# Kernel optimization log

Measured on AMD Instinct MI355X. Metric: run time of the kernel, lower is better.

Reference implementation:

```python
import jax, jax.numpy as jnp
import numpy as np

NUM_HEADS = 4

def setup_inputs() -> dict:
    key = jax.random.key(0)
    ks = jax.random.split(key, 5)
    B, N, C = 2, 4096, 256
    s = 0.02
    return {
        "x": jax.random.normal(ks[0], (B, N, C), dtype=jnp.float32),
        "qkv_w": jax.random.normal(ks[1], (3 * C, C), dtype=jnp.float32) * s,
        "qkv_b": jax.random.normal(ks[2], (3 * C,), dtype=jnp.float32) * s,
        "out_w": jax.random.normal(ks[3], (C, C), dtype=jnp.float32) * s,
        "out_b": jax.random.normal(ks[4], (C,), dtype=jnp.float32) * s,
    }

def reference(x, qkv_w, qkv_b, out_w, out_b):
    # x: [B, N, C]; manual multi-head self-attention (eval mode, dropout off)
    B, N, C = x.shape
    H = NUM_HEADS
    D = C // H
    qkv = x @ qkv_w.T + qkv_b                      # [B, N, 3C]
    qkv = qkv.reshape(B, N, 3, H, D)
    qkv = jnp.transpose(qkv, (2, 0, 3, 1, 4))      # [3, B, H, N, D]
    q, k, v = qkv[0], qkv[1], qkv[2]
    scale = D ** -0.5
    attn = jnp.einsum('bhnd,bhmd->bhnm', q, k) * scale  # [B, H, N, N]
    attn = jax.nn.softmax(attn, axis=-1)
    out = jnp.einsum('bhnm,bhmd->bhnd', attn, v)   # [B, H, N, D]
    out = jnp.transpose(out, (0, 2, 1, 3)).reshape(B, N, C)
    return out @ out_w.T + out_b
```

## Files before the change

### kernel.cpp

```cpp
#include <hip/hip_runtime.h>

typedef __bf16 bf16x8 __attribute__((ext_vector_type(8)));
typedef float f32x4 __attribute__((ext_vector_type(4)));

#define MFMA_BF16(a, b, c) __builtin_amdgcn_mfma_f32_16x16x32_bf16((a), (b), (c), 0, 0, 0)

#define C1 0.18033688f

static __device__ __forceinline__ unsigned short f2bf(float f) {
    unsigned int u = __float_as_uint(f);
    unsigned int r = (u + 0x7fffu + ((u >> 16) & 1u)) >> 16;
    return (unsigned short)r;
}
static __device__ __forceinline__ float bf2f(unsigned short us) {
    return __uint_as_float(((unsigned int)us) << 16);
}
static __device__ __forceinline__ float exp2_hw(float x) {
    float r;
    asm("v_exp_f32 %0, %1" : "=v"(r) : "v"(x));
    return r;
}
static __device__ __forceinline__ unsigned pack_rh(float a, float b) {
    return __byte_perm(__float_as_uint(a) + 0x8000u, __float_as_uint(b) + 0x8000u, 0x7632);
}
static __device__ __forceinline__ void gload16(const void* g, void* l) {
    __builtin_amdgcn_global_load_lds(
        (const __attribute__((address_space(1))) unsigned int*)g,
        (__attribute__((address_space(3))) unsigned int*)l, 16, 0, 0);
}

static __device__ __forceinline__ void conv_seg(const void* src, unsigned short* dst, int n,
                                                int lb, bool f32) {
#pragma unroll
    for (int j = 0; j < 4; j++) {
        int idx = lb * 1024 + j * 256 + (int)threadIdx.x;
        if (idx < n) {
            dst[idx] = f32 ? f2bf(((const float*)src)[idx]) : ((const unsigned short*)src)[idx];
        }
    }
}

__global__ __launch_bounds__(256) void convert_kernel(
    const void* __restrict__ x, const void* __restrict__ qw, const void* __restrict__ qb,
    const void* __restrict__ ow, const void* __restrict__ ob,
    unsigned short* __restrict__ xb, unsigned short* __restrict__ qwb,
    unsigned short* __restrict__ qbb, unsigned short* __restrict__ owb,
    unsigned short* __restrict__ obb, int* __restrict__ flag) {
    __shared__ int tot;
    if (threadIdx.x == 0) tot = 0;
    __syncthreads();
    {
        unsigned short v = ((const unsigned short*)x)[threadIdx.x];
        int e = (v >> 7) & 0xFF;
        if (e >= 195) atomicAdd(&tot, 1);
    }
    __syncthreads();
    const bool f32 = (tot >= 8);
    if (blockIdx.x == 0 && threadIdx.x == 0) flag[0] = f32 ? 1 : 0;

    const int bid = blockIdx.x;
    if (bid < 2048)       conv_seg(x,  xb,  2097152, bid,        f32);
    else if (bid < 2240)  conv_seg(qw, qwb, 196608,  bid - 2048, f32);
    else if (bid < 2241)  conv_seg(qb, qbb, 768,     bid - 2240, f32);
    else if (bid < 2305)  conv_seg(ow, owb, 65536,   bid - 2241, f32);
    else                  conv_seg(ob, obb, 256,     bid - 2305, f32);
}

template <int BM, bool QKV>
__global__ __launch_bounds__(256) void gemm_kernel(
    const unsigned short* __restrict__ A, const unsigned short* __restrict__ W,
    const unsigned short* __restrict__ bias, unsigned short* __restrict__ Cb,
    float* __restrict__ Cf, const int* __restrict__ flag,
    unsigned short* __restrict__ Vt, int Nout) {
    constexpr int K = 256;
    constexpr int WPM = BM / 64;
    constexpr int IA = BM / 32;
    constexpr int ABYT = BM * 128;
    __shared__ __align__(16) char sm[2 * ABYT + 16384];

    const int tid = threadIdx.x;
    const int lane = tid & 63;
    const int wv = tid >> 6;
    const int m16 = lane & 15;
    const int quad = lane >> 4;
    const int bm = blockIdx.x * BM;
    const int bn = blockIdx.y * 64;

    int ago[IA], alo[IA];
#pragma unroll
    for (int i = 0; i < IA; i++) {
        const int c = wv * (IA * 64) + i * 64 + lane;
        const int r = c >> 3, g = (c & 7) ^ (r & 7);
        ago[i] = r * (K * 2) + g * 16;
        alo[i] = c * 16;
    }
    int bgo[2], blo[2];
#pragma unroll
    for (int i = 0; i < 2; i++) {
        const int c = wv * 128 + i * 64 + lane;
        const int r = c >> 3, g = (c & 7) ^ (r & 7);
        bgo[i] = r * (K * 2) + g * 16;
        blo[i] = c * 16;
    }
    int aro[WPM][2], bro[4][2];
#pragma unroll
    for (int mb = 0; mb < WPM; mb++)
#pragma unroll
        for (int ks = 0; ks < 2; ks++) {
            const int row = wv * (WPM * 16) + mb * 16 + m16;
            aro[mb][ks] = row * 64 + ((4 * ks + quad) ^ (m16 & 7)) * 8;
        }
#pragma unroll
    for (int t = 0; t < 4; t++)
#pragma unroll
        for (int ks = 0; ks < 2; ks++) {
            const int row = t * 16 + m16;
            bro[t][ks] = row * 64 + ((4 * ks + quad) ^ (m16 & 7)) * 8;
        }

    const char* ag = (const char*)(A + (size_t)bm * K);
    const char* bg = (const char*)(W + (size_t)bn * K);

#pragma unroll
    for (int i = 0; i < IA; i++) gload16(ag + ago[i], sm + alo[i]);
#pragma unroll
    for (int i = 0; i < 2; i++) gload16(bg + bgo[i], sm + 2 * ABYT + blo[i]);

    f32x4 acc[WPM][4] = {};
#pragma unroll
    for (int kb = 0; kb < 4; kb++) {
        __syncthreads();
        const int cur = kb & 1;
        if (kb < 3) {
            ag += 128;
            bg += 128;
            char* Adst = sm + (cur ^ 1) * ABYT;
            char* Bdst = sm + 2 * ABYT + (cur ^ 1) * 8192;
#pragma unroll
            for (int i = 0; i < IA; i++) gload16(ag + ago[i], Adst + alo[i]);
#pragma unroll
            for (int i = 0; i < 2; i++) gload16(bg + bgo[i], Bdst + blo[i]);
        }
        const unsigned short* Alds = (const unsigned short*)(sm + cur * ABYT);
        const unsigned short* Blds = (const unsigned short*)(sm + 2 * ABYT + cur * 8192);
#pragma unroll
        for (int ks = 0; ks < 2; ks++) {
            bf16x8 bfr[4];
#pragma unroll
            for (int t = 0; t < 4; t++) bfr[t] = *(const bf16x8*)(Blds + bro[t][ks]);
#pragma unroll
            for (int mb = 0; mb < WPM; mb++) {
                const bf16x8 af = *(const bf16x8*)(Alds + aro[mb][ks]);
#pragma unroll
                for (int t = 0; t < 4; t++) acc[mb][t] = MFMA_BF16(af, bfr[t], acc[mb][t]);
            }
        }
    }

    const bool outf = (!QKV) && (flag != nullptr) && (*flag != 0);
#pragma unroll
    for (int mb = 0; mb < WPM; mb++) {
        const int row0 = bm + wv * (WPM * 16) + mb * 16 + quad * 4;
#pragma unroll
        for (int t = 0; t < 4; t++) {
            const int col = bn + t * 16 + m16;
            const float bv = bf2f(bias[col]);
            float v[4];
#pragma unroll
            for (int r = 0; r < 4; r++) v[r] = acc[mb][t][r] + bv;
            if (QKV) {
                if (col < 256) {
#pragma unroll
                    for (int r = 0; r < 4; r++)
                        Cb[(size_t)(row0 + r) * 768 + col] = f2bf(v[r] * C1);
                } else if (col < 512) {
#pragma unroll
                    for (int r = 0; r < 4; r++)
                        Cb[(size_t)(row0 + r) * 768 + col] = f2bf(v[r]);
                } else {
                    const int hh = (col - 512) >> 6, d = (col - 512) & 63;
                    const int bb = row0 >> 12, n0 = row0 & 4095;
                    uint2 w2;
                    w2.x = pack_rh(v[0], v[1]);
                    w2.y = pack_rh(v[2], v[3]);
                    *(uint2*)&Vt[((size_t)((bb * 4 + hh) * 64 + d)) * 4096 + n0] = w2;
                }
            } else {
                if (outf) {
#pragma unroll
                    for (int r = 0; r < 4; r++) Cf[(size_t)(row0 + r) * Nout + col] = v[r];
                } else {
#pragma unroll
                    for (int r = 0; r < 4; r++) Cb[(size_t)(row0 + r) * Nout + col] = f2bf(v[r]);
                }
            }
        }
    }
}

__global__ __launch_bounds__(256) void attn_kernel(
    const unsigned short* __restrict__ qkv, const unsigned short* __restrict__ Vt,
    unsigned short* __restrict__ attn, unsigned short* __restrict__ Opart,
    float* __restrict__ ml, int nsplit, int iters) {
    const int N = 4096, C3 = 768;
    __shared__ __align__(16) char sm[65536];

    const int tid = threadIdx.x;
    const int lane = tid & 63;
    const int wv = tid >> 6;
    const int m16 = lane & 15;
    const int quad = lane >> 4;

    const int bh = blockIdx.x & 7;
    const int qt = (blockIdx.x >> 3) & 63;
    const int kvs = blockIdx.x >> 9;
    const int b = bh >> 2, h = bh & 3;

    bf16x8 qf[4][2];
#pragma unroll
    for (int j = 0; j < 4; j++)
#pragma unroll
        for (int ks = 0; ks < 2; ks++)
            qf[j][ks] = *(const bf16x8*)(qkv + ((size_t)b * N + qt * 64 + j * 16 + m16) * C3 +
                                         h * 64 + ks * 32 + quad * 8);

    int kgo[4], vgo[4], klo[4], vlo[4];
#pragma unroll
    for (int i = 0; i < 4; i++) {
        const int c = wv * 256 + i * 64 + lane;
        const int r = c >> 3, g = (c & 7) ^ (r & 7);
        kgo[i] = r * 1536 + g * 16;
        klo[i] = c * 16;
        const int d = c >> 4, gg = (c & 15) ^ (d & 15);
        vgo[i] = d * 8192 + gg * 16;
        vlo[i] = c * 16;
    }
    int kro[2][2], vro[4], pwo[2][4], pro[4];
#pragma unroll
    for (int mb = 0; mb < 2; mb++)
#pragma unroll
        for (int ks = 0; ks < 2; ks++) {
            const int row = wv * 32 + mb * 16 + m16;
            kro[mb][ks] = row * 64 + ((4 * ks + quad) ^ (m16 & 7)) * 8;
        }
#pragma unroll
    for (int t = 0; t < 4; t++) vro[t] = (t * 16 + m16) * 128 + ((wv * 4 + quad) ^ m16) * 8;
#pragma unroll
    for (int mb = 0; mb < 2; mb++)
#pragma unroll
        for (int j = 0; j < 4; j++)
            pwo[mb][j] = wv * 2048 + (j * 16 + m16) * 32 +
                         ((2 * mb + (quad >> 1)) ^ (m16 & 3)) * 8 + (quad & 1) * 4;
#pragma unroll
    for (int j = 0; j < 4; j++)
        pro[j] = wv * 2048 + (j * 16 + m16) * 32 + (quad ^ (m16 & 3)) * 8;

    const char* kgp = (const char*)(qkv + (size_t)b * N * C3 + 256 + h * 64) +
                      (size_t)(kvs * iters) * 128 * 1536;
    const char* vgp = (const char*)(Vt + (size_t)bh * 64 * N) + (size_t)(kvs * iters) * 256;

#pragma unroll
    for (int i = 0; i < 4; i++) {
        gload16(kgp + kgo[i], sm + klo[i]);
        gload16(vgp + vgo[i], sm + 32768 + vlo[i]);
    }

    f32x4 o[4][4] = {};
    float lac[4] = {0.f, 0.f, 0.f, 0.f};

    for (int kt = 0; kt < iters; ++kt) {
        __syncthreads();
        const int cur = kt & 1;
        if (kt + 1 < iters) {
            kgp += 128 * 1536;
            vgp += 256;
            char* Kdst = sm + (cur ^ 1) * 16384;
            char* Vdst = sm + 32768 + (cur ^ 1) * 16384;
#pragma unroll
            for (int i = 0; i < 4; i++) {
                gload16(kgp + kgo[i], Kdst + klo[i]);
                gload16(vgp + vgo[i], Vdst + vlo[i]);
            }
        }
        unsigned short* Kb = (unsigned short*)(sm + cur * 16384);
        const unsigned short* Vb = (const unsigned short*)(sm + 32768 + cur * 16384);

        f32x4 s[2][4] = {};
#pragma unroll
        for (int mb = 0; mb < 2; mb++)
#pragma unroll
            for (int ks = 0; ks < 2; ks++) {
                const bf16x8 ka = *(const bf16x8*)(Kb + kro[mb][ks]);
#pragma unroll
                for (int j = 0; j < 4; j++) s[mb][j] = MFMA_BF16(ka, qf[j][ks], s[mb][j]);
            }

#pragma unroll
        for (int mb = 0; mb < 2; mb++)
#pragma unroll
            for (int j = 0; j < 4; j++) {
                const float p0 = exp2_hw(s[mb][j][0]);
                const float p1 = exp2_hw(s[mb][j][1]);
                const float p2 = exp2_hw(s[mb][j][2]);
                const float p3 = exp2_hw(s[mb][j][3]);
                lac[j] += (p0 + p1) + (p2 + p3);
                uint2 w;
                w.x = pack_rh(p0, p1);
                w.y = pack_rh(p2, p3);
                *(uint2*)(Kb + pwo[mb][j]) = w;
            }
        asm volatile("s_waitcnt lgkmcnt(0)" ::: "memory");

        bf16x8 pa[4];
#pragma unroll
        for (int j = 0; j < 4; j++) pa[j] = *(const bf16x8*)(Kb + pro[j]);
#pragma unroll
        for (int t = 0; t < 4; t++) {
            const bf16x8 vb = *(const bf16x8*)(Vb + vro[t]);
#pragma unroll
            for (int j = 0; j < 4; j++) o[j][t] = MFMA_BF16(pa[j], vb, o[j][t]);
        }
    }

#pragma unroll
    for (int j = 0; j < 4; j++) {
        lac[j] += __shfl_xor(lac[j], 16);
        lac[j] += __shfl_xor(lac[j], 32);
    }
    __syncthreads();
    float* Ored = (float*)sm;
    float* lsum = (float*)(sm + 16384);
    if (quad == 0) {
#pragma unroll
        for (int j = 0; j < 4; j++) lsum[wv * 64 + j * 16 + m16] = lac[j];
    }
    const int row = tid >> 4;
    const int col = (tid & 15) * 4;
#pragma unroll
    for (int j = 0; j < 4; j++) {
#pragma unroll
        for (int t = 0; t < 4; t++)
#pragma unroll
            for (int r = 0; r < 4; r++)
                Ored[(wv * 16 + quad * 4 + r) * 64 + t * 16 + m16] = o[j][t][r];
        __syncthreads();
        f32x4 sum = *(f32x4*)&Ored[row * 64 + col];
        sum += *(f32x4*)&Ored[1024 + row * 64 + col];
        sum += *(f32x4*)&Ored[2048 + row * 64 + col];
        sum += *(f32x4*)&Ored[3072 + row * 64 + col];
        const float lq = lsum[j * 16 + row] + lsum[64 + j * 16 + row] +
                         lsum[128 + j * 16 + row] + lsum[192 + j * 16 + row];
        const int n = qt * 64 + j * 16 + row;
        if (nsplit == 1) {
            const float inv = 1.0f / lq;
            uint2 w;
            w.x = pack_rh(sum[0] * inv, sum[1] * inv);
            w.y = pack_rh(sum[2] * inv, sum[3] * inv);
            *(uint2*)&attn[((size_t)b * N + n) * 256 + h * 64 + col] = w;
        } else {
            uint2 w;
            w.x = pack_rh(sum[0], sum[1]);
            w.y = pack_rh(sum[2], sum[3]);
            *(uint2*)&Opart[(((size_t)(kvs * 8 + bh)) * N + n) * 64 + col] = w;
            if ((tid & 15) == 0) {
                float2 mv;
                mv.x = 0.0f;
                mv.y = lq;
                *(float2*)&ml[(((size_t)(kvs * 8 + bh)) * N + n) * 2] = mv;
            }
        }
        __syncthreads();
    }
}

__global__ __launch_bounds__(256) void merge_kernel(
    const unsigned short* __restrict__ Opart, const float* __restrict__ ml,
    unsigned short* __restrict__ attn, int nsplit) {
    const int N = 4096;
    const int gt = blockIdx.x * 256 + threadIdx.x;
    const int d = gt & 63;
    const int row = gt >> 6;
    const int bh = row >> 12;
    const int n = row & 4095;
    const int b = bh >> 2, h = bh & 3;

    float m = -INFINITY;
    for (int j = 0; j < nsplit; j++) m = fmaxf(m, ml[((size_t)(j * 8 + bh) * N + n) * 2]);
    float acc = 0.0f, l = 0.0f;
    for (int j = 0; j < nsplit; j++) {
        const size_t rbase = (size_t)(j * 8 + bh) * N + n;
        const float2 mv = *(const float2*)(&ml[rbase * 2]);
        const float w = exp2_hw(mv.x - m);
        l += w * mv.y;
        acc += w * bf2f(Opart[rbase * 64 + d]);
    }
    attn[((size_t)b * N + n) * 256 + h * 64 + d] = f2bf(acc / l);
}

extern "C" void kernel_launch(void* const* d_in, const int* in_sizes, int n_in,
                              void* d_out, int out_size, void* d_ws, size_t ws_size,
                              hipStream_t stream) {
    const int B = 2, N = 4096, H = 4;
    const int M = B * N;

    char* wsb = (char*)d_ws;
    int* flag = (int*)wsb;
    unsigned short* xb      = (unsigned short*)(wsb + 64);
    unsigned short* qwb     = xb + 2097152;
    unsigned short* qbb     = qwb + 196608;
    unsigned short* owb     = qbb + 768;
    unsigned short* obb     = owb + 65536;
    unsigned short* qkv_ws  = obb + 256;
    unsigned short* Vt_ws   = qkv_ws + 6291456;
    unsigned short* attn_ws = Vt_ws + 2097152;
    unsigned short* Opart   = attn_ws + 2097152;

    const size_t used = 64 + 2ull * (2097152 + 196608 + 768 + 65536 + 256 +
                                     6291456 + 2097152 + 2097152);
    const size_t perS = 8ull * 4096 * 64 * 2 + 8ull * 4096 * 2 * 4;
    int S = 1;
    if (ws_size >= used + 2 * perS + 128) S = 2;
    float* ml = (float*)(((uintptr_t)(Opart + (size_t)S * 2097152) + 15) & ~(uintptr_t)15);
    const int iters = N / (128 * S);

    convert_kernel<<<2306, 256, 0, stream>>>(d_in[0], d_in[1], d_in[2], d_in[3], d_in[4],
                                             xb, qwb, qbb, owb, obb, flag);

    gemm_kernel<128, true><<<dim3(M / 128, 768 / 64), 256, 0, stream>>>(
        xb, qwb, qbb, qkv_ws, nullptr, nullptr, Vt_ws, 768);

    attn_kernel<<<512 * S, 256, 0, stream>>>(qkv_ws, Vt_ws, attn_ws, Opart, ml, S, iters);

    if (S > 1) {
        merge_kernel<<<8 * N * 64 / 256, 256, 0, stream>>>(Opart, ml, attn_ws, S);
    }

    gemm_kernel<64, false><<<dim3(M / 64, 256 / 64), 256, 0, stream>>>(
        attn_ws, owb, obb, (unsigned short*)d_out, (float*)d_out, flag, nullptr, 256);
}
```

Baseline: 157.1 us.

## Load V fragments directly from global to registers and allow four-way KV split

V tiles are no longer staged through shared memory. Each lane now loads its V MFMA operand straight from the transposed V buffer in global memory at the start of every iteration, which halves LDS use to 32 KB and may allow more blocks per CU. The KV split factor can also rise to 4 when the workspace is large enough, giving more blocks and fewer iterations per block. In exchange, the V loads are not prefetched, so their global latency sits exposed inside each iteration, and the merge kernel has more partial results to combine.

```diff
diff --git a/kernel.cpp b/kernel.cpp
--- a/kernel.cpp
+++ b/kernel.cpp
@@ -203,7 +203,7 @@
     unsigned short* __restrict__ attn, unsigned short* __restrict__ Opart,
     float* __restrict__ ml, int nsplit, int iters) {
     const int N = 4096, C3 = 768;
-    __shared__ __align__(16) char sm[65536];
+    __shared__ __align__(16) char sm[32768];
 
     const int tid = threadIdx.x;
     const int lane = tid & 63;
@@ -224,18 +224,15 @@
             qf[j][ks] = *(const bf16x8*)(qkv + ((size_t)b * N + qt * 64 + j * 16 + m16) * C3 +
                                          h * 64 + ks * 32 + quad * 8);
 
-    int kgo[4], vgo[4], klo[4], vlo[4];
+    int kgo[4], klo[4];
 #pragma unroll
     for (int i = 0; i < 4; i++) {
         const int c = wv * 256 + i * 64 + lane;
         const int r = c >> 3, g = (c & 7) ^ (r & 7);
         kgo[i] = r * 1536 + g * 16;
         klo[i] = c * 16;
-        const int d = c >> 4, gg = (c & 15) ^ (d & 15);
-        vgo[i] = d * 8192 + gg * 16;
-        vlo[i] = c * 16;
-    }
-    int kro[2][2], vro[4], pwo[2][4], pro[4];
+    }
+    int kro[2][2], pwo[2][4], pro[4];
 #pragma unroll
     for (int mb = 0; mb < 2; mb++)
 #pragma unroll
@@ -244,8 +241,6 @@
             kro[mb][ks] = row * 64 + ((4 * ks + quad) ^ (m16 & 7)) * 8;
         }
 #pragma unroll
-    for (int t = 0; t < 4; t++) vro[t] = (t * 16 + m16) * 128 + ((wv * 4 + quad) ^ m16) * 8;
-#pragma unroll
     for (int mb = 0; mb < 2; mb++)
 #pragma unroll
         for (int j = 0; j < 4; j++)
@@ -257,13 +252,14 @@
 
     const char* kgp = (const char*)(qkv + (size_t)b * N * C3 + 256 + h * 64) +
                       (size_t)(kvs * iters) * 128 * 1536;
-    const char* vgp = (const char*)(Vt + (size_t)bh * 64 * N) + (size_t)(kvs * iters) * 256;
-
-#pragma unroll
-    for (int i = 0; i < 4; i++) {
-        gload16(kgp + kgo[i], sm + klo[i]);
-        gload16(vgp + vgo[i], sm + 32768 + vlo[i]);
-    }
+    const unsigned short* vptr[4];
+#pragma unroll
+    for (int t = 0; t < 4; t++)
+        vptr[t] = Vt + ((size_t)bh * 64 + t * 16 + m16) * N + kvs * iters * 128 +
+                  wv * 32 + quad * 8;
+
+#pragma unroll
+    for (int i = 0; i < 4; i++) gload16(kgp + kgo[i], sm + klo[i]);
 
     f32x4 o[4][4] = {};
     float lac[4] = {0.f, 0.f, 0.f, 0.f};
@@ -271,19 +267,20 @@
     for (int kt = 0; kt < iters; ++kt) {
         __syncthreads();
         const int cur = kt & 1;
+
+        bf16x8 vb[4];
+#pragma unroll
+        for (int t = 0; t < 4; t++) {
+            vb[t] = *(const bf16x8*)(vptr[t]);
+            vptr[t] += 128;
+        }
         if (kt + 1 < iters) {
             kgp += 128 * 1536;
-            vgp += 256;
             char* Kdst = sm + (cur ^ 1) * 16384;
-            char* Vdst = sm + 32768 + (cur ^ 1) * 16384;
-#pragma unroll
-            for (int i = 0; i < 4; i++) {
-                gload16(kgp + kgo[i], Kdst + klo[i]);
-                gload16(vgp + vgo[i], Vdst + vlo[i]);
-            }
+#pragma unroll
+            for (int i = 0; i < 4; i++) gload16(kgp + kgo[i], Kdst + klo[i]);
         }
         unsigned short* Kb = (unsigned short*)(sm + cur * 16384);
-        const unsigned short* Vb = (const unsigned short*)(sm + 32768 + cur * 16384);
 
         f32x4 s[2][4] = {};
 #pragma unroll
@@ -316,9 +313,8 @@
         for (int j = 0; j < 4; j++) pa[j] = *(const bf16x8*)(Kb + pro[j]);
 #pragma unroll
         for (int t = 0; t < 4; t++) {
-            const bf16x8 vb = *(const bf16x8*)(Vb + vro[t]);
-#pragma unroll
-            for (int j = 0; j < 4; j++) o[j][t] = MFMA_BF16(pa[j], vb, o[j][t]);
+#pragma unroll
+            for (int j = 0; j < 4; j++) o[j][t] = MFMA_BF16(pa[j], vb[t], o[j][t]);
         }
     }
 
@@ -419,7 +415,8 @@
                                      6291456 + 2097152 + 2097152);
     const size_t perS = 8ull * 4096 * 64 * 2 + 8ull * 4096 * 2 * 4;
     int S = 1;
-    if (ws_size >= used + 2 * perS + 128) S = 2;
+    if (ws_size >= used + 4 * perS + 128) S = 4;
+    else if (ws_size >= used + 2 * perS + 128) S = 2;
     float* ml = (float*)(((uintptr_t)(Opart + (size_t)S * 2097152) + 15) & ~(uintptr_t)15);
     const int iters = N / (128 * S);
 
```

New measurement: 168.9 us. 1.08x slower.
